# Kernel optimization log

Hardware: AMD Instinct MI355X
Metric: run time of the kernel (lower is better)

The kernel has to match this reference:

```python
import jax, jax.numpy as jnp
import numpy as np

N_NODES = 100000
N_EDGES = 3200000
FEAT = 64  # pos(32) + vel(32)
OUT_DIM = 2


def setup_inputs() -> dict:
    key = jax.random.key(0)
    k1, k2, k3, k4, k5, k6, k7, k8 = jax.random.split(key, 8)
    pos = jax.random.normal(k1, (N_NODES, 32), dtype=jnp.float32)
    vel = jax.random.normal(k2, (N_NODES, 32), dtype=jnp.float32)
    edge_index = jax.random.randint(k3, (2, N_EDGES), 0, N_NODES, dtype=jnp.int64 if jax.config.jax_enable_x64 else jnp.int32)
    s = 1.0 / np.sqrt(FEAT)
    W_rel = jax.random.uniform(k4, (FEAT, FEAT), jnp.float32, -s, s)
    b_rel = jax.random.uniform(k5, (FEAT,), jnp.float32, -s, s)
    W_root = jax.random.uniform(k6, (FEAT, FEAT), jnp.float32, -s, s)
    W_pred = jax.random.uniform(k7, (FEAT, OUT_DIM), jnp.float32, -s, s)
    b_pred = jax.random.uniform(k8, (OUT_DIM,), jnp.float32, -s, s)
    return {"pos": pos, "vel": vel, "edge_index": edge_index,
            "W_rel": W_rel, "b_rel": b_rel, "W_root": W_root,
            "W_pred": W_pred, "b_pred": b_pred}


def reference(pos, vel, edge_index, W_rel, b_rel, W_root, W_pred, b_pred):
    # h = cat([pos, vel], -1)  -> [N, 64]
    h = jnp.concatenate([pos, vel], axis=-1)
    src, dst = edge_index[0], edge_index[1]
    # GraphConv (PyG, aggr='add'): out_i = lin_rel(sum_{j->i} h_j) + lin_root(h_i)
    msgs = h[src]  # [E, 64] irregular gather
    agg = jax.ops.segment_sum(msgs, dst, num_segments=N_NODES)  # [N, 64]
    conv_out = agg @ W_rel + b_rel + h @ W_root
    # lin_pred
    return conv_out @ W_pred + b_pred
```

## Files before the change

### kernel.cpp

```cpp
#include <hip/hip_runtime.h>

#define N_NODES 100000
#define N_EDGES 3200000
#define FEAT 64
#define OUT_DIM 2

#define K_DST 64
#define DST_SZ 1568
#define NPART 8
#define PART_SZ 12500
#define NSUB (K_DST * NPART)
#define CAP_SUB 6724
#define NB 400
#define EPB (N_EDGES / NB)
#define BT 1024


__global__ __launch_bounds__(256) void node_kernel(const float* __restrict__ pos,
                                                   const float* __restrict__ vel,
                                                   const float* __restrict__ W_rel,
                                                   const float* __restrict__ b_rel,
                                                   const float* __restrict__ W_root,
                                                   const float* __restrict__ W_pred,
                                                   const float* __restrict__ b_pred,
                                                   unsigned* __restrict__ y,
                                                   float* __restrict__ out,
                                                   int* __restrict__ gcount) {
    __shared__ float sM[258];
    int t = threadIdx.x;

    if (blockIdx.x == 0)
        for (int i = t; i < NSUB; i += 256) gcount[i] = 0;

    {
        const float* W = (t < 128) ? W_rel : W_root;
        int k = (t & 127) >> 1, o = t & 1;
        float acc = 0.f;
        #pragma unroll
        for (int f = 0; f < FEAT; ++f) acc += W[k * FEAT + f] * W_pred[f * OUT_DIM + o];
        sM[t] = acc;
        if (t < OUT_DIM) {
            float b = b_pred[t];
            #pragma unroll
            for (int f = 0; f < FEAT; ++f) b += b_rel[f] * W_pred[f * OUT_DIM + t];
            sM[256 + t] = b;
        }
    }
    __syncthreads();

    int n = blockIdx.x * 256 + t;
    if (n >= N_NODES) return;

    const float4* p4 = (const float4*)(pos + (size_t)n * 32);
    const float4* v4 = (const float4*)(vel + (size_t)n * 32);
    float h[FEAT];
    #pragma unroll
    for (int i = 0; i < 8; ++i) {
        float4 a = p4[i];
        h[i * 4 + 0] = a.x; h[i * 4 + 1] = a.y; h[i * 4 + 2] = a.z; h[i * 4 + 3] = a.w;
    }
    #pragma unroll
    for (int i = 0; i < 8; ++i) {
        float4 a = v4[i];
        h[32 + i * 4 + 0] = a.x; h[32 + i * 4 + 1] = a.y; h[32 + i * 4 + 2] = a.z; h[32 + i * 4 + 3] = a.w;
    }

    float rel0 = 0.f, rel1 = 0.f, ro0 = 0.f, ro1 = 0.f;
    #pragma unroll
    for (int k = 0; k < FEAT; ++k) {
        float hk = h[k];
        rel0 += hk * sM[2 * k + 0];
        rel1 += hk * sM[2 * k + 1];
        ro0  += hk * sM[128 + 2 * k + 0];
        ro1  += hk * sM[128 + 2 * k + 1];
    }
    unsigned bx = __float_as_uint(rel0);
    unsigned by = __float_as_uint(rel1);
    bx += 0x7FFFu + ((bx >> 16) & 1u);
    by += 0x7FFFu + ((by >> 16) & 1u);
    y[n] = (bx >> 16) | (by & 0xFFFF0000u);
    ((float2*)out)[n] = make_float2(ro0 + sM[256], ro1 + sM[257]);
}

__global__ __launch_bounds__(BT) void binscatter_kernel(const int* __restrict__ edges,
                                                        int* __restrict__ gcount,
                                                        unsigned* __restrict__ scat) {
    __shared__ int hist[NSUB];
    __shared__ int cum[NSUB + 1];
    __shared__ int base[NSUB];
    __shared__ int rpos[NSUB];
    __shared__ unsigned sortbuf[EPB];

    int t = threadIdx.x;
    for (int i = t; i < NSUB; i += BT) hist[i] = 0;
    __syncthreads();

    const int4* s4 = (const int4*)(edges) + blockIdx.x * (EPB / 4);
    const int4* d4 = (const int4*)(edges + N_EDGES) + blockIdx.x * (EPB / 4);
    int4 sreg[2], dreg[2];
    bool valid[2];
    #pragma unroll
    for (int r = 0; r < 2; ++r) {
        int i = t + r * BT;
        valid[r] = (i < EPB / 4);
        if (valid[r]) { sreg[r] = s4[i]; dreg[r] = d4[i]; }
    }

    #pragma unroll
    for (int r = 0; r < 2; ++r) {
        if (!valid[r]) continue;
        int4 s = sreg[r];
        int4 d = dreg[r];
        atomicAdd(&hist[((unsigned)d.x / DST_SZ) * NPART + (unsigned)s.x / PART_SZ], 1);
        atomicAdd(&hist[((unsigned)d.y / DST_SZ) * NPART + (unsigned)s.y / PART_SZ], 1);
        atomicAdd(&hist[((unsigned)d.z / DST_SZ) * NPART + (unsigned)s.z / PART_SZ], 1);
        atomicAdd(&hist[((unsigned)d.w / DST_SZ) * NPART + (unsigned)s.w / PART_SZ], 1);
    }
    __syncthreads();

    for (int i = t; i < NSUB; i += BT) base[i] = atomicAdd(&gcount[i], hist[i]);
    if (t < 64) {
        int lo = t * 8;
        int vals[8];
        int lsum = 0;
        #pragma unroll
        for (int j = 0; j < 8; ++j) { int v = hist[lo + j]; vals[j] = lsum; lsum += v; }
        int x = lsum;
        #pragma unroll
        for (int d = 1; d < 64; d <<= 1) {
            int up = __shfl_up(x, d);
            if (t >= d) x += up;
        }
        int excl = x - lsum;
        #pragma unroll
        for (int j = 0; j < 8; ++j) { cum[lo + j] = excl + vals[j]; rpos[lo + j] = excl + vals[j]; }
        if (t == 63) cum[NSUB] = excl + lsum;
    }
    __syncthreads();

    #pragma unroll
    for (int r = 0; r < 2; ++r) {
        if (!valid[r]) continue;
        int4 s = sreg[r];
        int4 d = dreg[r];
        int kk, p, dl;
        kk = (unsigned)d.x / DST_SZ; dl = d.x - kk * DST_SZ;
        p = atomicAdd(&rpos[kk * NPART + (unsigned)s.x / PART_SZ], 1);
        sortbuf[p] = (unsigned)s.x | ((unsigned)dl << 17);
        kk = (unsigned)d.y / DST_SZ; dl = d.y - kk * DST_SZ;
        p = atomicAdd(&rpos[kk * NPART + (unsigned)s.y / PART_SZ], 1);
        sortbuf[p] = (unsigned)s.y | ((unsigned)dl << 17);
        kk = (unsigned)d.z / DST_SZ; dl = d.z - kk * DST_SZ;
        p = atomicAdd(&rpos[kk * NPART + (unsigned)s.z / PART_SZ], 1);
        sortbuf[p] = (unsigned)s.z | ((unsigned)dl << 17);
        kk = (unsigned)d.w / DST_SZ; dl = d.w - kk * DST_SZ;
        p = atomicAdd(&rpos[kk * NPART + (unsigned)s.w / PART_SZ], 1);
        sortbuf[p] = (unsigned)s.w | ((unsigned)dl << 17);
    }
    __syncthreads();

    int wid = t >> 6, lane = t & 63;
    for (int k = wid; k < NSUB; k += BT / 64) {
        int s0 = cum[k], s1 = cum[k + 1], b = base[k];
        for (int j = s0 + lane; j < s1; j += 64) {
            int p = b + (j - s0);
            if (p < CAP_SUB) scat[(size_t)k * CAP_SUB + p] = sortbuf[j];
        }
    }
}

__global__ __launch_bounds__(BT, 8) void accum_partial_kernel(const unsigned* __restrict__ scat,
                                                              const int* __restrict__ gcount,
                                                              const unsigned* __restrict__ y,
                                                              unsigned* __restrict__ partial) {
    __shared__ unsigned yl[PART_SZ];
    __shared__ float accx[DST_SZ];
    __shared__ float accy[DST_SZ];

    const int t = threadIdx.x;
    const int sub = blockIdx.x;
    const int p = sub & (NPART - 1);

    int c = gcount[sub];
    if (c > CAP_SUB) c = CAP_SUB;
    const int nq = (c + 3) >> 2;

    const uint4* y4 = (const uint4*)(y) + p * (PART_SZ / 4);
    uint4 q0 = y4[t];
    uint4 q1 = y4[t + BT];
    uint4 q2 = y4[t + 2 * BT];
    uint4 q3;
    const bool s3 = t < (PART_SZ / 4 - 3 * BT);
    if (s3) q3 = y4[t + 3 * BT];

    const uint4* sc4 = (const uint4*)(scat + (size_t)sub * CAP_SUB);
    uint4 e0, e1;
    const bool g0 = t < nq, g1 = (t + BT) < nq;
    if (g0) e0 = sc4[t];
    if (g1) e1 = sc4[t + BT];

    for (int i = t; i < DST_SZ; i += BT) { accx[i] = 0.f; accy[i] = 0.f; }

    uint4* yl4 = (uint4*)yl;
    yl4[t] = q0;
    yl4[t + BT] = q1;
    yl4[t + 2 * BT] = q2;
    if (s3) yl4[t + 3 * BT] = q3;
    __syncthreads();

    const int pbase = p * PART_SZ;
    if (g0) {
        int eidx = t << 2;
        unsigned v0 = yl[(int)(e0.x & 0x1FFFF) - pbase];
        unsigned v1 = yl[(int)(e0.y & 0x1FFFF) - pbase];
        unsigned v2 = yl[(int)(e0.z & 0x1FFFF) - pbase];
        unsigned v3 = yl[(int)(e0.w & 0x1FFFF) - pbase];
        if (eidx + 0 < c) { atomicAdd(&accx[e0.x >> 17], __uint_as_float(v0 << 16)); atomicAdd(&accy[e0.x >> 17], __uint_as_float(v0 & 0xFFFF0000u)); }
        if (eidx + 1 < c) { atomicAdd(&accx[e0.y >> 17], __uint_as_float(v1 << 16)); atomicAdd(&accy[e0.y >> 17], __uint_as_float(v1 & 0xFFFF0000u)); }
        if (eidx + 2 < c) { atomicAdd(&accx[e0.z >> 17], __uint_as_float(v2 << 16)); atomicAdd(&accy[e0.z >> 17], __uint_as_float(v2 & 0xFFFF0000u)); }
        if (eidx + 3 < c) { atomicAdd(&accx[e0.w >> 17], __uint_as_float(v3 << 16)); atomicAdd(&accy[e0.w >> 17], __uint_as_float(v3 & 0xFFFF0000u)); }
    }
    if (g1) {
        int eidx = (t + BT) << 2;
        unsigned v0 = yl[(int)(e1.x & 0x1FFFF) - pbase];
        unsigned v1 = yl[(int)(e1.y & 0x1FFFF) - pbase];
        unsigned v2 = yl[(int)(e1.z & 0x1FFFF) - pbase];
        unsigned v3 = yl[(int)(e1.w & 0x1FFFF) - pbase];
        if (eidx + 0 < c) { atomicAdd(&accx[e1.x >> 17], __uint_as_float(v0 << 16)); atomicAdd(&accy[e1.x >> 17], __uint_as_float(v0 & 0xFFFF0000u)); }
        if (eidx + 1 < c) { atomicAdd(&accx[e1.y >> 17], __uint_as_float(v1 << 16)); atomicAdd(&accy[e1.y >> 17], __uint_as_float(v1 & 0xFFFF0000u)); }
        if (eidx + 2 < c) { atomicAdd(&accx[e1.z >> 17], __uint_as_float(v2 << 16)); atomicAdd(&accy[e1.z >> 17], __uint_as_float(v2 & 0xFFFF0000u)); }
        if (eidx + 3 < c) { atomicAdd(&accx[e1.w >> 17], __uint_as_float(v3 << 16)); atomicAdd(&accy[e1.w >> 17], __uint_as_float(v3 & 0xFFFF0000u)); }
    }
    __syncthreads();

    for (int i = t; i < DST_SZ; i += BT) {
        unsigned bx = __float_as_uint(accx[i]);
        unsigned by = __float_as_uint(accy[i]);
        bx += 0x7FFFu + ((bx >> 16) & 1u);
        by += 0x7FFFu + ((by >> 16) & 1u);
        partial[(size_t)sub * DST_SZ + i] = (bx >> 16) | (by & 0xFFFF0000u);
    }
}

__global__ __launch_bounds__(BT) void merge_kernel(const unsigned* __restrict__ partial,
                                                   float* __restrict__ out) {
    int n = blockIdx.x * BT + threadIdx.x;
    if (n >= N_NODES) return;
    unsigned kd = (unsigned)n / DST_SZ;
    int dl = n - kd * DST_SZ;

    float sx = 0.f, sy = 0.f;
    #pragma unroll
    for (int p = 0; p < NPART; ++p) {
        unsigned v = partial[((size_t)(kd * NPART + p)) * DST_SZ + dl];
        sx += __uint_as_float(v << 16);
        sy += __uint_as_float(v & 0xFFFF0000u);
    }
    float2* o2 = (float2*)out;
    float2 cv = o2[n];
    cv.x += sx;
    cv.y += sy;
    o2[n] = cv;
}

extern "C" void kernel_launch(void* const* d_in, const int* in_sizes, int n_in,
                              void* d_out, int out_size, void* d_ws, size_t ws_size,
                              hipStream_t stream) {
    const float* pos    = (const float*)d_in[0];
    const float* vel    = (const float*)d_in[1];
    const int*   edges  = (const int*)d_in[2];
    const float* W_rel  = (const float*)d_in[3];
    const float* b_rel  = (const float*)d_in[4];
    const float* W_root = (const float*)d_in[5];
    const float* W_pred = (const float*)d_in[6];
    const float* b_pred = (const float*)d_in[7];
    float* out = (float*)d_out;

    char* ws = (char*)d_ws;
    unsigned* y       = (unsigned*)(ws + 2048);
    int*      gcount  = (int*)(ws + 402048);
    unsigned* scat    = (unsigned*)(ws + 404096);
    unsigned* partial = (unsigned*)(ws + 14174848);

    int node_blocks = (N_NODES + 255) / 256;
    node_kernel<<<node_blocks, 256, 0, stream>>>(pos, vel, W_rel, b_rel, W_root,
                                                 W_pred, b_pred, y, out, gcount);

    binscatter_kernel<<<NB, BT, 0, stream>>>(edges, gcount, scat);

    accum_partial_kernel<<<NSUB, BT, 0, stream>>>(scat, gcount, y, partial);

    merge_kernel<<<98, BT, 0, stream>>>(partial, out);
}
```

Before: 162.3 us.

## Fuse merge into accumulate via last-block arrival counter; use 256 binscatter blocks

The separate merge kernel is removed. Each destination group now has an atomic arrival counter, and the last of its 8 partition blocks sums the partials and updates the output. Binscatter drops from 400 to 256 blocks, so each block handles 12500 edges (three or four int4 loads per thread, issued before the first barrier). This saves one kernel launch and gives each block more work, at the cost of threadfence/atomic overhead and a serialized tail merge in 64 blocks. The larger per-block sortbuf also reduces LDS occupancy.

```diff
diff --git a/kernel.cpp b/kernel.cpp
--- a/kernel.cpp
+++ b/kernel.cpp
@@ -11,8 +11,10 @@
 #define PART_SZ 12500
 #define NSUB (K_DST * NPART)
 #define CAP_SUB 6724
-#define NB 400
+#define NB 256
 #define EPB (N_EDGES / NB)
+#define NQ (EPB / 4)
+#define V3LIM (NQ - 3 * 1024)
 #define BT 1024
 
 
@@ -25,12 +27,15 @@
                                                    const float* __restrict__ b_pred,
                                                    unsigned* __restrict__ y,
                                                    float* __restrict__ out,
-                                                   int* __restrict__ gcount) {
+                                                   int* __restrict__ gcount,
+                                                   int* __restrict__ arrive) {
     __shared__ float sM[258];
     int t = threadIdx.x;
 
-    if (blockIdx.x == 0)
+    if (blockIdx.x == 0) {
         for (int i = t; i < NSUB; i += 256) gcount[i] = 0;
+        if (t < K_DST) arrive[t] = 0;
+    }
 
     {
         const float* W = (t < 128) ? W_rel : W_root;
@@ -93,29 +98,23 @@
 
     int t = threadIdx.x;
     for (int i = t; i < NSUB; i += BT) hist[i] = 0;
-    __syncthreads();
-
-    const int4* s4 = (const int4*)(edges) + blockIdx.x * (EPB / 4);
-    const int4* d4 = (const int4*)(edges + N_EDGES) + blockIdx.x * (EPB / 4);
-    int4 sreg[2], dreg[2];
-    bool valid[2];
-    #pragma unroll
-    for (int r = 0; r < 2; ++r) {
-        int i = t + r * BT;
-        valid[r] = (i < EPB / 4);
-        if (valid[r]) { sreg[r] = s4[i]; dreg[r] = d4[i]; }
-    }
-
-    #pragma unroll
-    for (int r = 0; r < 2; ++r) {
-        if (!valid[r]) continue;
-        int4 s = sreg[r];
-        int4 d = dreg[r];
-        atomicAdd(&hist[((unsigned)d.x / DST_SZ) * NPART + (unsigned)s.x / PART_SZ], 1);
-        atomicAdd(&hist[((unsigned)d.y / DST_SZ) * NPART + (unsigned)s.y / PART_SZ], 1);
-        atomicAdd(&hist[((unsigned)d.z / DST_SZ) * NPART + (unsigned)s.z / PART_SZ], 1);
-        atomicAdd(&hist[((unsigned)d.w / DST_SZ) * NPART + (unsigned)s.w / PART_SZ], 1);
-    }
+
+    const int4* s4 = (const int4*)(edges) + blockIdx.x * NQ;
+    const int4* d4 = (const int4*)(edges + N_EDGES) + blockIdx.x * NQ;
+    int4 s0 = s4[t], s1 = s4[t + BT], s2 = s4[t + 2 * BT];
+    int4 d0 = d4[t], d1 = d4[t + BT], d2 = d4[t + 2 * BT];
+    const bool v3 = t < V3LIM;
+    int4 s3, d3;
+    if (v3) { s3 = s4[t + 3 * BT]; d3 = d4[t + 3 * BT]; }
+    __syncthreads();
+
+    #define HISTADD(dd, ss) \
+        atomicAdd(&hist[((unsigned)(dd) / DST_SZ) * NPART + (unsigned)(ss) / PART_SZ], 1)
+    HISTADD(d0.x, s0.x); HISTADD(d0.y, s0.y); HISTADD(d0.z, s0.z); HISTADD(d0.w, s0.w);
+    HISTADD(d1.x, s1.x); HISTADD(d1.y, s1.y); HISTADD(d1.z, s1.z); HISTADD(d1.w, s1.w);
+    HISTADD(d2.x, s2.x); HISTADD(d2.y, s2.y); HISTADD(d2.z, s2.z); HISTADD(d2.w, s2.w);
+    if (v3) { HISTADD(d3.x, s3.x); HISTADD(d3.y, s3.y); HISTADD(d3.z, s3.z); HISTADD(d3.w, s3.w); }
+    #undef HISTADD
     __syncthreads();
 
     for (int i = t; i < NSUB; i += BT) base[i] = atomicAdd(&gcount[i], hist[i]);
@@ -138,48 +137,43 @@
     }
     __syncthreads();
 
-    #pragma unroll
-    for (int r = 0; r < 2; ++r) {
-        if (!valid[r]) continue;
-        int4 s = sreg[r];
-        int4 d = dreg[r];
-        int kk, p, dl;
-        kk = (unsigned)d.x / DST_SZ; dl = d.x - kk * DST_SZ;
-        p = atomicAdd(&rpos[kk * NPART + (unsigned)s.x / PART_SZ], 1);
-        sortbuf[p] = (unsigned)s.x | ((unsigned)dl << 17);
-        kk = (unsigned)d.y / DST_SZ; dl = d.y - kk * DST_SZ;
-        p = atomicAdd(&rpos[kk * NPART + (unsigned)s.y / PART_SZ], 1);
-        sortbuf[p] = (unsigned)s.y | ((unsigned)dl << 17);
-        kk = (unsigned)d.z / DST_SZ; dl = d.z - kk * DST_SZ;
-        p = atomicAdd(&rpos[kk * NPART + (unsigned)s.z / PART_SZ], 1);
-        sortbuf[p] = (unsigned)s.z | ((unsigned)dl << 17);
-        kk = (unsigned)d.w / DST_SZ; dl = d.w - kk * DST_SZ;
-        p = atomicAdd(&rpos[kk * NPART + (unsigned)s.w / PART_SZ], 1);
-        sortbuf[p] = (unsigned)s.w | ((unsigned)dl << 17);
-    }
+    #define SCATTER(dd, ss) { \
+        unsigned kk = (unsigned)(dd) / DST_SZ; \
+        int dl = (dd) - (int)(kk * DST_SZ); \
+        int p = atomicAdd(&rpos[kk * NPART + (unsigned)(ss) / PART_SZ], 1); \
+        sortbuf[p] = (unsigned)(ss) | ((unsigned)dl << 17); }
+    SCATTER(d0.x, s0.x); SCATTER(d0.y, s0.y); SCATTER(d0.z, s0.z); SCATTER(d0.w, s0.w);
+    SCATTER(d1.x, s1.x); SCATTER(d1.y, s1.y); SCATTER(d1.z, s1.z); SCATTER(d1.w, s1.w);
+    SCATTER(d2.x, s2.x); SCATTER(d2.y, s2.y); SCATTER(d2.z, s2.z); SCATTER(d2.w, s2.w);
+    if (v3) { SCATTER(d3.x, s3.x); SCATTER(d3.y, s3.y); SCATTER(d3.z, s3.z); SCATTER(d3.w, s3.w); }
+    #undef SCATTER
     __syncthreads();
 
     int wid = t >> 6, lane = t & 63;
     for (int k = wid; k < NSUB; k += BT / 64) {
-        int s0 = cum[k], s1 = cum[k + 1], b = base[k];
-        for (int j = s0 + lane; j < s1; j += 64) {
-            int p = b + (j - s0);
+        int a0 = cum[k], a1 = cum[k + 1], b = base[k];
+        for (int j = a0 + lane; j < a1; j += 64) {
+            int p = b + (j - a0);
             if (p < CAP_SUB) scat[(size_t)k * CAP_SUB + p] = sortbuf[j];
         }
     }
 }
 
-__global__ __launch_bounds__(BT, 8) void accum_partial_kernel(const unsigned* __restrict__ scat,
-                                                              const int* __restrict__ gcount,
-                                                              const unsigned* __restrict__ y,
-                                                              unsigned* __restrict__ partial) {
+__global__ __launch_bounds__(BT, 8) void accum_merge_kernel(const unsigned* __restrict__ scat,
+                                                            const int* __restrict__ gcount,
+                                                            const unsigned* __restrict__ y,
+                                                            unsigned* __restrict__ partial,
+                                                            int* __restrict__ arrive,
+                                                            float* __restrict__ out) {
     __shared__ unsigned yl[PART_SZ];
     __shared__ float accx[DST_SZ];
     __shared__ float accy[DST_SZ];
+    __shared__ int lastFlag;
 
     const int t = threadIdx.x;
     const int sub = blockIdx.x;
     const int p = sub & (NPART - 1);
+    const int kd = sub >> 3;
 
     int c = gcount[sub];
     if (c > CAP_SUB) c = CAP_SUB;
@@ -240,27 +234,34 @@
         by += 0x7FFFu + ((by >> 16) & 1u);
         partial[(size_t)sub * DST_SZ + i] = (bx >> 16) | (by & 0xFFFF0000u);
     }
-}
-
-__global__ __launch_bounds__(BT) void merge_kernel(const unsigned* __restrict__ partial,
-                                                   float* __restrict__ out) {
-    int n = blockIdx.x * BT + threadIdx.x;
-    if (n >= N_NODES) return;
-    unsigned kd = (unsigned)n / DST_SZ;
-    int dl = n - kd * DST_SZ;
-
-    float sx = 0.f, sy = 0.f;
-    #pragma unroll
-    for (int p = 0; p < NPART; ++p) {
-        unsigned v = partial[((size_t)(kd * NPART + p)) * DST_SZ + dl];
-        sx += __uint_as_float(v << 16);
-        sy += __uint_as_float(v & 0xFFFF0000u);
-    }
+
+    __threadfence();
+    if (t == 0) {
+        int prev = atomicAdd(&arrive[kd], 1);
+        lastFlag = (prev == NPART - 1);
+    }
+    __syncthreads();
+    if (!lastFlag) return;
+
+    __threadfence();
+    const unsigned* pb = partial + (size_t)kd * NPART * DST_SZ;
     float2* o2 = (float2*)out;
-    float2 cv = o2[n];
-    cv.x += sx;
-    cv.y += sy;
-    o2[n] = cv;
+    for (int i = t; i < DST_SZ; i += BT) {
+        int n = kd * DST_SZ + i;
+        if (n < N_NODES) {
+            float sx = 0.f, sy = 0.f;
+            #pragma unroll
+            for (int pp = 0; pp < NPART; ++pp) {
+                unsigned v = pb[(size_t)pp * DST_SZ + i];
+                sx += __uint_as_float(v << 16);
+                sy += __uint_as_float(v & 0xFFFF0000u);
+            }
+            float2 cv = o2[n];
+            cv.x += sx;
+            cv.y += sy;
+            o2[n] = cv;
+        }
+    }
 }
 
 extern "C" void kernel_launch(void* const* d_in, const int* in_sizes, int n_in,
@@ -281,14 +282,13 @@
     int*      gcount  = (int*)(ws + 402048);
     unsigned* scat    = (unsigned*)(ws + 404096);
     unsigned* partial = (unsigned*)(ws + 14174848);
+    int*      arrive  = (int*)(ws + 17386112);
 
     int node_blocks = (N_NODES + 255) / 256;
     node_kernel<<<node_blocks, 256, 0, stream>>>(pos, vel, W_rel, b_rel, W_root,
-                                                 W_pred, b_pred, y, out, gcount);
+                                                 W_pred, b_pred, y, out, gcount, arrive);
 
     binscatter_kernel<<<NB, BT, 0, stream>>>(edges, gcount, scat);
 
-    accum_partial_kernel<<<NSUB, BT, 0, stream>>>(scat, gcount, y, partial);
-
-    merge_kernel<<<98, BT, 0, stream>>>(partial, out);
-}
+    accum_merge_kernel<<<NSUB, BT, 0, stream>>>(scat, gcount, y, partial, arrive, out);
+}
```

After: 315.4 us. +94.3%, slower.
